# Performance work log

Hardware: AMD Instinct MI355X
Metric: run time of the kernel (lower is better)

## Reference

```python
import jax, jax.numpy as jnp
import numpy as np

T, B, N = 2048, 32, 1024   # time, batch, dan_hidden_size
H = 8                      # multihead_size
N2 = 128                   # attention_hidden_size
K = N // H                 # N_H = 128 per-head dim
K2 = N2 // H               # N2_H = 16 per-head attention dim


def setup_inputs() -> dict:
    key = jax.random.key(0)
    ks = jax.random.split(key, 10)
    s_n = 1.0 / np.sqrt(N)
    s_k = 1.0 / np.sqrt(K)
    s_k2 = 1.0 / np.sqrt(K2)
    return {
        "hyp": jax.random.normal(ks[0], (T, B, N), dtype=jnp.float32),
        # H independent per-head linears N -> K, stacked: (H, K, N)
        "Wmh": jax.random.uniform(ks[1], (H, K, N), minval=-s_n, maxval=s_n, dtype=jnp.float32),
        "bmh": jax.random.uniform(ks[2], (H, K), minval=-s_n, maxval=s_n, dtype=jnp.float32),
        # shared W: K -> K2
        "W": jax.random.uniform(ks[3], (K2, K), minval=-s_k, maxval=s_k, dtype=jnp.float32),
        "bW": jax.random.uniform(ks[4], (K2,), minval=-s_k, maxval=s_k, dtype=jnp.float32),
        # shared W_m: K -> K2
        "Wm": jax.random.uniform(ks[5], (K2, K), minval=-s_k, maxval=s_k, dtype=jnp.float32),
        "bWm": jax.random.uniform(ks[6], (K2,), minval=-s_k, maxval=s_k, dtype=jnp.float32),
        # shared W_h: K2 -> 1
        "Wh": jax.random.uniform(ks[7], (K2,), minval=-s_k2, maxval=s_k2, dtype=jnp.float32),
        "bWh": jax.random.uniform(ks[8], (), minval=-s_k2, maxval=s_k2, dtype=jnp.float32),
        "dan_hidden_size": N,
        "attention_hidden_size": N2,
        "multihead_size": H,
    }


def reference(hyp, Wmh, bmh, W, bW, Wm, bWm, Wh, bWh,
              dan_hidden_size, attention_hidden_size, multihead_size):
    # Per-head projections, all heads at once: (B, T, H, K)
    X = jnp.einsum('tbn,hkn->bthk', hyp, Wmh) + bmh
    # mean over time (original x.mean(0)): (B, H, K)
    m = X.mean(axis=1)
    # tanh-gated additive scoring: (B, T, H, K2)
    g = jnp.tanh(jnp.einsum('bthk,qk->bthq', X, W) + bW) \
        * jnp.tanh(jnp.einsum('bhk,qk->bhq', m, Wm) + bWm)[:, None]
    # scalar score per (b, t, h), softmax over time
    s = jnp.einsum('bthq,q->bth', g, Wh) + bWh
    a = jax.nn.softmax(s, axis=1)                       # (B, T, H)
    # attention-weighted sum over time: (B, H, K)
    c = jnp.einsum('bth,bthk->bhk', a, X)
    # concat heads along feature dim (head-major order, matches torch.cat)
    Bsz = c.shape[0]
    return c.reshape(Bsz, -1)                            # (B, N)
```

## Files before the change

kernel.cpp:

```cpp
#include <hip/hip_runtime.h>
#include <hip/hip_bf16.h>

#define T_DIM 2048
#define B_DIM 32
#define N_DIM 1024
#define H_DIM 8
#define K_DIM 128
#define Q_DIM 16

typedef __bf16 bf16x8 __attribute__((ext_vector_type(8)));
typedef __bf16 bf16x4 __attribute__((ext_vector_type(4)));
typedef float  f32x4  __attribute__((ext_vector_type(4)));

__device__ inline bf16x8 cvt8(float4 a, float4 b) {
    bf16x8 r;
    r[0] = (__bf16)a.x; r[1] = (__bf16)a.y; r[2] = (__bf16)a.z; r[3] = (__bf16)a.w;
    r[4] = (__bf16)b.x; r[5] = (__bf16)b.y; r[6] = (__bf16)b.z; r[7] = (__bf16)b.w;
    return r;
}

__global__ __launch_bounds__(256)
void cvt_f32_bf16(const float* __restrict__ s, __bf16* __restrict__ d)
{
    const long i = ((long)blockIdx.x * 256 + threadIdx.x) * 8;
    float4 a = *(const float4*)(s + i);
    float4 b = *(const float4*)(s + i + 4);
    *(bf16x8*)(d + i) = cvt8(a, b);
}

__global__ __launch_bounds__(512, 2)
void gemm_x_8ph(const __bf16* __restrict__ A, const __bf16* __restrict__ Bw,
                const float* __restrict__ bias, __bf16* __restrict__ X,
                float* __restrict__ mpart)
{
    __shared__ __bf16 lds[2][2][16384];

    const int tid  = threadIdx.x;
    const int lane = tid & 63;
    const int w    = tid >> 6;
    const int wm   = w >> 2;
    const int wn   = w & 3;

    const int bid  = blockIdx.x;
    const int wgid = (bid & 7) * 128 + (bid >> 3);
    const int bm   = wgid >> 2;
    const int bn   = wgid & 3;
    const long row0 = (long)bm * 256;
    const long col0 = (long)bn * 256;

    const int srow = w * 8 + (lane >> 3);
    const int scol = ((lane & 7) ^ (lane >> 3)) * 8;
    const __bf16* Ag = A  + (row0 + srow) * 1024 + scol;
    const __bf16* Bg = Bw + (col0 + srow) * 1024 + scol;
    const int ldst = w * 512;

    auto stage = [&](int kt, int sl) {
        const long ko = (long)kt * 64;
        #pragma unroll
        for (int j = 0; j < 4; ++j)
            __builtin_amdgcn_global_load_lds(
                (const __attribute__((address_space(1))) void*)(Ag + (long)j * 65536 + ko),
                (__attribute__((address_space(3))) void*)(&lds[sl][0][j * 4096 + ldst]),
                16, 0, 0);
        #pragma unroll
        for (int j = 0; j < 4; ++j)
            __builtin_amdgcn_global_load_lds(
                (const __attribute__((address_space(1))) void*)(Bg + (long)j * 65536 + ko),
                (__attribute__((address_space(3))) void*)(&lds[sl][1][j * 4096 + ldst]),
                16, 0, 0);
    };

    const int fr = lane & 15;
    const int g2 = lane >> 4;
    const int x7 = lane & 7;

    f32x4 acc[8][4];
    #pragma unroll
    for (int i = 0; i < 8; ++i)
        #pragma unroll
        for (int j = 0; j < 4; ++j)
            acc[i][j] = f32x4{0.f, 0.f, 0.f, 0.f};

    stage(0, 0);
    stage(1, 1);
    asm volatile("s_waitcnt vmcnt(8)" ::: "memory");
    __builtin_amdgcn_s_barrier();

    #pragma unroll 1
    for (int i = 0; i < 16; ++i) {
        const int s = i & 1;
        const __bf16* Al = &lds[s][0][0];
        const __bf16* Bl = &lds[s][1][0];

        bf16x8 a0[4], a0h[4], a1[4], a1h[4], b0[4], b1[4];

        #pragma unroll
        for (int mi = 0; mi < 4; ++mi) {
            const int row = wm * 128 + mi * 16 + fr;
            a0[mi] = *(const bf16x8*)(Al + row * 64 + ((g2) ^ x7) * 8);
        }
        #pragma unroll
        for (int ni = 0; ni < 4; ++ni) {
            const int row = wn * 64 + ni * 16 + fr;
            b0[ni] = *(const bf16x8*)(Bl + row * 64 + ((g2) ^ x7) * 8);
        }
        __builtin_amdgcn_s_barrier();
        __builtin_amdgcn_s_setprio(1);
        #pragma unroll
        for (int mi = 0; mi < 4; ++mi)
            #pragma unroll
            for (int ni = 0; ni < 4; ++ni)
                acc[mi][ni] = __builtin_amdgcn_mfma_f32_16x16x32_bf16(b0[ni], a0[mi], acc[mi][ni], 0, 0, 0);
        __builtin_amdgcn_s_setprio(0);
        __builtin_amdgcn_s_barrier();

        #pragma unroll
        for (int mi = 0; mi < 4; ++mi) {
            const int row = wm * 128 + mi * 16 + fr;
            a0h[mi] = *(const bf16x8*)(Al + row * 64 + ((4 + g2) ^ x7) * 8);
        }
        #pragma unroll
        for (int ni = 0; ni < 4; ++ni) {
            const int row = wn * 64 + ni * 16 + fr;
            b1[ni] = *(const bf16x8*)(Bl + row * 64 + ((4 + g2) ^ x7) * 8);
        }
        __builtin_amdgcn_s_barrier();
        __builtin_amdgcn_s_setprio(1);
        #pragma unroll
        for (int mi = 0; mi < 4; ++mi)
            #pragma unroll
            for (int ni = 0; ni < 4; ++ni)
                acc[mi][ni] = __builtin_amdgcn_mfma_f32_16x16x32_bf16(b1[ni], a0h[mi], acc[mi][ni], 0, 0, 0);
        __builtin_amdgcn_s_setprio(0);
        __builtin_amdgcn_s_barrier();

        #pragma unroll
        for (int mi = 0; mi < 4; ++mi) {
            const int row = wm * 128 + (mi + 4) * 16 + fr;
            a1[mi]  = *(const bf16x8*)(Al + row * 64 + ((g2    ) ^ x7) * 8);
            a1h[mi] = *(const bf16x8*)(Al + row * 64 + ((4 + g2) ^ x7) * 8);
        }
        __builtin_amdgcn_s_barrier();
        __builtin_amdgcn_s_setprio(1);
        #pragma unroll
        for (int mi = 0; mi < 4; ++mi)
            #pragma unroll
            for (int ni = 0; ni < 4; ++ni)
                acc[mi + 4][ni] = __builtin_amdgcn_mfma_f32_16x16x32_bf16(b0[ni], a1[mi], acc[mi + 4][ni], 0, 0, 0);
        __builtin_amdgcn_s_setprio(0);
        __builtin_amdgcn_s_barrier();

        if (i < 14) stage(i + 2, s);
        __builtin_amdgcn_s_barrier();
        __builtin_amdgcn_s_setprio(1);
        #pragma unroll
        for (int mi = 0; mi < 4; ++mi)
            #pragma unroll
            for (int ni = 0; ni < 4; ++ni)
                acc[mi + 4][ni] = __builtin_amdgcn_mfma_f32_16x16x32_bf16(b1[ni], a1h[mi], acc[mi + 4][ni], 0, 0, 0);
        __builtin_amdgcn_s_setprio(0);
        if (i < 14) { asm volatile("s_waitcnt vmcnt(8)" ::: "memory"); }
        else        { asm volatile("s_waitcnt vmcnt(0)" ::: "memory"); }
        __builtin_amdgcn_s_barrier();
    }

    const int g4 = lane >> 4;
    const long colb = col0 + wn * 64 + g4 * 4;

    float4 bias4[4];
    #pragma unroll
    for (int ni = 0; ni < 4; ++ni)
        bias4[ni] = *(const float4*)(bias + colb + ni * 16);

    f32x4 msum[2][4];
    #pragma unroll
    for (int bh = 0; bh < 2; ++bh)
        #pragma unroll
        for (int ni = 0; ni < 4; ++ni)
            msum[bh][ni] = f32x4{0.f, 0.f, 0.f, 0.f};

    #pragma unroll
    for (int mi = 0; mi < 8; ++mi) {
        const long row = row0 + wm * 128 + mi * 16 + fr;
        #pragma unroll
        for (int ni = 0; ni < 4; ++ni) {
            f32x4 xv;
            xv[0] = acc[mi][ni][0] + bias4[ni].x;
            xv[1] = acc[mi][ni][1] + bias4[ni].y;
            xv[2] = acc[mi][ni][2] + bias4[ni].z;
            xv[3] = acc[mi][ni][3] + bias4[ni].w;
            bf16x4 xb;
            xb[0] = (__bf16)xv[0]; xb[1] = (__bf16)xv[1];
            xb[2] = (__bf16)xv[2]; xb[3] = (__bf16)xv[3];
            *(bf16x4*)(X + row * 1024 + colb + ni * 16) = xb;
            msum[mi & 1][ni] += xv;
        }
    }

    float* ldsf = (float*)&lds[0][0][0];
    __syncthreads();
    if (wm == 1) {
        #pragma unroll
        for (int bh = 0; bh < 2; ++bh)
            #pragma unroll
            for (int ni = 0; ni < 4; ++ni)
                *(f32x4*)(ldsf + (bh * 16 + fr) * 256 + wn * 64 + ni * 16 + g4 * 4) = msum[bh][ni];
    }
    __syncthreads();
    if (wm == 0) {
        #pragma unroll
        for (int bh = 0; bh < 2; ++bh) {
            const int b = bh * 16 + fr;
            #pragma unroll
            for (int ni = 0; ni < 4; ++ni) {
                f32x4 other = *(const f32x4*)(ldsf + b * 256 + wn * 64 + ni * 16 + g4 * 4);
                f32x4 tot = msum[bh][ni] + other;
                *(f32x4*)(mpart + ((long)bm * 32 + b) * 1024 + colb + ni * 16) = tot;
            }
        }
    }
}

__global__ __launch_bounds__(256)
void gate2_k(const float* __restrict__ mpart, const float* __restrict__ Wm,
             const float* __restrict__ bWm, float* __restrict__ g2)
{
    __shared__ float mrow[1024];
    const int b = blockIdx.x;
    const int j4 = threadIdx.x * 4;
    f32x4 s = f32x4{0.f, 0.f, 0.f, 0.f};
    for (int bm = 0; bm < 256; ++bm)
        s += *(const f32x4*)(mpart + ((long)bm * 32 + b) * 1024 + j4);
    mrow[j4 + 0] = s[0] * (1.0f / 2048.0f);
    mrow[j4 + 1] = s[1] * (1.0f / 2048.0f);
    mrow[j4 + 2] = s[2] * (1.0f / 2048.0f);
    mrow[j4 + 3] = s[3] * (1.0f / 2048.0f);
    __syncthreads();
    if (threadIdx.x < 128) {
        const int h = threadIdx.x >> 4;
        const int q = threadIdx.x & 15;
        float d = bWm[q];
        #pragma unroll 8
        for (int k = 0; k < 128; ++k) d += mrow[h * 128 + k] * Wm[q * 128 + k];
        g2[(b * 8 + h) * 16 + q] = tanhf(d);
    }
}

__global__ __launch_bounds__(256)
void scores_k(const __bf16* __restrict__ X, const float* __restrict__ W,
              const float* __restrict__ bW, const float* __restrict__ g2,
              const float* __restrict__ Wh, const float* __restrict__ bWh,
              float* __restrict__ sbuf)
{
    const int tid   = threadIdx.x;
    const int lane  = tid & 63;
    const int w     = tid >> 6;
    const int gw    = blockIdx.x * 4 + w;
    const int rbase = gw * 16;
    const int q     = lane & 15;
    const int g4    = lane >> 4;

    bf16x8 bfr[4];
    #pragma unroll
    for (int c = 0; c < 4; ++c) {
        const float* wp = W + q * 128 + c * 32 + g4 * 8;
        float4 w0 = *(const float4*)wp;
        float4 w1 = *(const float4*)(wp + 4);
        bfr[c] = cvt8(w0, w1);
    }
    const __bf16* xp = X + (long)(rbase + q) * 128 + g4 * 8;
    bf16x8 afr[4];
    #pragma unroll
    for (int c = 0; c < 4; ++c) afr[c] = *(const bf16x8*)(xp + c * 32);

    f32x4 acc = f32x4{0.f, 0.f, 0.f, 0.f};
    #pragma unroll
    for (int c = 0; c < 4; ++c)
        acc = __builtin_amdgcn_mfma_f32_16x16x32_bf16(afr[c], bfr[c], acc, 0, 0, 0);

    const float whq  = Wh[q];
    const float bWv  = bW[q];
    const float bWhv = *bWh;
    #pragma unroll
    for (int r = 0; r < 4; ++r) {
        const int row = rbase + g4 * 4 + r;
        const int h   = row & 7;
        const int bt  = row >> 3;
        const int b   = bt & 31;
        const int t   = bt >> 5;
        float val = tanhf(acc[r] + bWv) * g2[(b * 8 + h) * 16 + q] * whq;
        val += __shfl_xor(val, 1);
        val += __shfl_xor(val, 2);
        val += __shfl_xor(val, 4);
        val += __shfl_xor(val, 8);
        if (q == 0) sbuf[(b * 8 + h) * 2048 + t] = val + bWhv;
    }
}

__global__ __launch_bounds__(256)
void softmax_k(float* __restrict__ s)
{
    __shared__ float red[256];
    const int bh = blockIdx.x;
    const int tid = threadIdx.x;
    float* row = s + bh * 2048;
    float4 v0 = *(const float4*)(row + tid * 8);
    float4 v1 = *(const float4*)(row + tid * 8 + 4);
    float v[8] = {v0.x, v0.y, v0.z, v0.w, v1.x, v1.y, v1.z, v1.w};
    float mx = v[0];
    #pragma unroll
    for (int i = 1; i < 8; ++i) mx = fmaxf(mx, v[i]);
    red[tid] = mx;
    __syncthreads();
    for (int st = 128; st > 0; st >>= 1) {
        if (tid < st) red[tid] = fmaxf(red[tid], red[tid + st]);
        __syncthreads();
    }
    mx = red[0];
    __syncthreads();
    float sum = 0.f;
    #pragma unroll
    for (int i = 0; i < 8; ++i) { v[i] = expf(v[i] - mx); sum += v[i]; }
    red[tid] = sum;
    __syncthreads();
    for (int st = 128; st > 0; st >>= 1) {
        if (tid < st) red[tid] += red[tid + st];
        __syncthreads();
    }
    const float inv = 1.0f / red[0];
    *(float4*)(row + tid * 8)     = make_float4(v[0] * inv, v[1] * inv, v[2] * inv, v[3] * inv);
    *(float4*)(row + tid * 8 + 4) = make_float4(v[4] * inv, v[5] * inv, v[6] * inv, v[7] * inv);
}

__global__ __launch_bounds__(256)
void wsum_k(const float* __restrict__ a, const __bf16* __restrict__ X,
            float* __restrict__ wpart)
{
    __shared__ float pk[8 * 128];
    const int bx = blockIdx.x;
    const int tc = bx & 7;
    const int bh = bx >> 3;
    const int b  = bh >> 3;
    const int h  = bh & 7;
    const int tid = threadIdx.x;
    const int kq = tid & 31;
    const int tr = tid >> 5;
    const float* ar = a + bh * 2048 + tc * 256;
    float a0 = 0.f, a1 = 0.f, a2 = 0.f, a3 = 0.f;
    #pragma unroll 4
    for (int i = tr; i < 256; i += 8) {
        const int t = tc * 256 + i;
        const float av = ar[i];
        bf16x4 xv = *(const bf16x4*)(X + (long)(t * 32 + b) * 1024 + h * 128 + kq * 4);
        a0 += av * (float)xv[0];
        a1 += av * (float)xv[1];
        a2 += av * (float)xv[2];
        a3 += av * (float)xv[3];
    }
    pk[tr * 128 + kq * 4 + 0] = a0;
    pk[tr * 128 + kq * 4 + 1] = a1;
    pk[tr * 128 + kq * 4 + 2] = a2;
    pk[tr * 128 + kq * 4 + 3] = a3;
    __syncthreads();
    if (tid < 128) {
        float s2 = 0.f;
        #pragma unroll
        for (int r = 0; r < 8; ++r) s2 += pk[r * 128 + tid];
        wpart[(long)bx * 128 + tid] = s2;
    }
}

__global__ __launch_bounds__(256)
void wsum_fin(const float* __restrict__ wpart, float* __restrict__ out)
{
    const int idx = blockIdx.x * 256 + threadIdx.x;
    const int k  = idx & 127;
    const int bh = idx >> 7;
    const int b  = bh >> 3;
    const int h  = bh & 7;
    float s = 0.f;
    #pragma unroll
    for (int tc = 0; tc < 8; ++tc) s += wpart[(bh * 8 + tc) * 128 + k];
    out[b * 1024 + h * 128 + k] = s;
}

extern "C" void kernel_launch(void* const* d_in, const int* in_sizes, int n_in,
                              void* d_out, int out_size, void* d_ws, size_t ws_size,
                              hipStream_t stream)
{
    const float* hyp = (const float*)d_in[0];
    const float* Wmh = (const float*)d_in[1];
    const float* bmh = (const float*)d_in[2];
    const float* W   = (const float*)d_in[3];
    const float* bW  = (const float*)d_in[4];
    const float* Wm  = (const float*)d_in[5];
    const float* bWm = (const float*)d_in[6];
    const float* Wh  = (const float*)d_in[7];
    const float* bWh = (const float*)d_in[8];
    float* out = (float*)d_out;

    char* ws = (char*)d_ws;
    const size_t SZ_X   = 134217728;
    const size_t SZ_AB  = 134217728;
    const size_t SZ_BB  = 2097152;
    const size_t SZ_MP  = 33554432;
    const size_t SZ_G2  = 16384;
    const size_t SZ_SB  = 2097152;

    size_t off = 0;
    __bf16* X     = (__bf16*)(ws + off); off += SZ_X;
    __bf16* Ab    = (__bf16*)(ws + off); off += SZ_AB;
    __bf16* Bb    = (__bf16*)(ws + off); off += SZ_BB;
    float*  mpart = (float*) (ws + off); off += SZ_MP;
    float*  g2    = (float*) (ws + off); off += SZ_G2;
    float*  sbuf  = (float*) (ws + off); off += SZ_SB;
    float*  wpart = (float*) (ws + off);

    cvt_f32_bf16<<<32768, 256, 0, stream>>>(hyp, Ab);
    cvt_f32_bf16<<<512,   256, 0, stream>>>(Wmh, Bb);
    gemm_x_8ph<<<1024, 512, 0, stream>>>(Ab, Bb, bmh, X, mpart);
    gate2_k<<<32, 256, 0, stream>>>(mpart, Wm, bWm, g2);
    scores_k<<<8192, 256, 0, stream>>>(X, W, bW, g2, Wh, bWh, sbuf);
    softmax_k<<<256, 256, 0, stream>>>(sbuf);
    wsum_k<<<2048, 256, 0, stream>>>(sbuf, X, wpart);
    wsum_fin<<<128, 256, 0, stream>>>(wpart, out);
}
```

Baseline: 346.7 us.

## Software-pipeline LDS fragment loads across MFMA phases and cut barriers

Restructures the GEMM main loop so the LDS fragment reads for the next phase are issued before the current MFMA block, and the first fragments of the next K-tile are prefetched from the other LDS buffer at the end of each iteration. The number of workgroup barriers per iteration drops from about eight to two, with an explicit lgkmcnt wait before the global-to-LDS staging overwrites the current buffer. The aim is to hide LDS latency behind matrix-core work and reduce synchronisation stalls. It raises register pressure from the fragments held across iterations, and ordering mistakes could cause LDS races.

```diff
diff --git a/kernel.cpp b/kernel.cpp
--- a/kernel.cpp
+++ b/kernel.cpp
@@ -86,25 +86,33 @@
     asm volatile("s_waitcnt vmcnt(8)" ::: "memory");
     __builtin_amdgcn_s_barrier();
 
+    bf16x8 a0[4], b0[4];
+    {
+        const __bf16* Al = &lds[0][0][0];
+        const __bf16* Bl = &lds[0][1][0];
+        #pragma unroll
+        for (int mi = 0; mi < 4; ++mi)
+            a0[mi] = *(const bf16x8*)(Al + (wm * 128 + mi * 16 + fr) * 64 + ((g2) ^ x7) * 8);
+        #pragma unroll
+        for (int ni = 0; ni < 4; ++ni)
+            b0[ni] = *(const bf16x8*)(Bl + (wn * 64 + ni * 16 + fr) * 64 + ((g2) ^ x7) * 8);
+    }
+
     #pragma unroll 1
     for (int i = 0; i < 16; ++i) {
         const int s = i & 1;
         const __bf16* Al = &lds[s][0][0];
         const __bf16* Bl = &lds[s][1][0];
 
-        bf16x8 a0[4], a0h[4], a1[4], a1h[4], b0[4], b1[4];
-
-        #pragma unroll
-        for (int mi = 0; mi < 4; ++mi) {
-            const int row = wm * 128 + mi * 16 + fr;
-            a0[mi] = *(const bf16x8*)(Al + row * 64 + ((g2) ^ x7) * 8);
-        }
-        #pragma unroll
-        for (int ni = 0; ni < 4; ++ni) {
-            const int row = wn * 64 + ni * 16 + fr;
-            b0[ni] = *(const bf16x8*)(Bl + row * 64 + ((g2) ^ x7) * 8);
-        }
-        __builtin_amdgcn_s_barrier();
+        bf16x8 a0h[4], a1[4], a1h[4], b1[4];
+
+        #pragma unroll
+        for (int mi = 0; mi < 4; ++mi)
+            a0h[mi] = *(const bf16x8*)(Al + (wm * 128 + mi * 16 + fr) * 64 + ((4 + g2) ^ x7) * 8);
+        #pragma unroll
+        for (int ni = 0; ni < 4; ++ni)
+            b1[ni] = *(const bf16x8*)(Bl + (wn * 64 + ni * 16 + fr) * 64 + ((4 + g2) ^ x7) * 8);
+
         __builtin_amdgcn_s_setprio(1);
         #pragma unroll
         for (int mi = 0; mi < 4; ++mi)
@@ -112,27 +120,6 @@
             for (int ni = 0; ni < 4; ++ni)
                 acc[mi][ni] = __builtin_amdgcn_mfma_f32_16x16x32_bf16(b0[ni], a0[mi], acc[mi][ni], 0, 0, 0);
         __builtin_amdgcn_s_setprio(0);
-        __builtin_amdgcn_s_barrier();
-
-        #pragma unroll
-        for (int mi = 0; mi < 4; ++mi) {
-            const int row = wm * 128 + mi * 16 + fr;
-            a0h[mi] = *(const bf16x8*)(Al + row * 64 + ((4 + g2) ^ x7) * 8);
-        }
-        #pragma unroll
-        for (int ni = 0; ni < 4; ++ni) {
-            const int row = wn * 64 + ni * 16 + fr;
-            b1[ni] = *(const bf16x8*)(Bl + row * 64 + ((4 + g2) ^ x7) * 8);
-        }
-        __builtin_amdgcn_s_barrier();
-        __builtin_amdgcn_s_setprio(1);
-        #pragma unroll
-        for (int mi = 0; mi < 4; ++mi)
-            #pragma unroll
-            for (int ni = 0; ni < 4; ++ni)
-                acc[mi][ni] = __builtin_amdgcn_mfma_f32_16x16x32_bf16(b1[ni], a0h[mi], acc[mi][ni], 0, 0, 0);
-        __builtin_amdgcn_s_setprio(0);
-        __builtin_amdgcn_s_barrier();
 
         #pragma unroll
         for (int mi = 0; mi < 4; ++mi) {
@@ -140,7 +127,18 @@
             a1[mi]  = *(const bf16x8*)(Al + row * 64 + ((g2    ) ^ x7) * 8);
             a1h[mi] = *(const bf16x8*)(Al + row * 64 + ((4 + g2) ^ x7) * 8);
         }
+        __builtin_amdgcn_s_setprio(1);
+        #pragma unroll
+        for (int mi = 0; mi < 4; ++mi)
+            #pragma unroll
+            for (int ni = 0; ni < 4; ++ni)
+                acc[mi][ni] = __builtin_amdgcn_mfma_f32_16x16x32_bf16(b1[ni], a0h[mi], acc[mi][ni], 0, 0, 0);
+        __builtin_amdgcn_s_setprio(0);
+
+        asm volatile("s_waitcnt lgkmcnt(0)" ::: "memory");
         __builtin_amdgcn_s_barrier();
+        if (i < 14) stage(i + 2, s);
+
         __builtin_amdgcn_s_setprio(1);
         #pragma unroll
         for (int mi = 0; mi < 4; ++mi)
@@ -148,20 +146,28 @@
             for (int ni = 0; ni < 4; ++ni)
                 acc[mi + 4][ni] = __builtin_amdgcn_mfma_f32_16x16x32_bf16(b0[ni], a1[mi], acc[mi + 4][ni], 0, 0, 0);
         __builtin_amdgcn_s_setprio(0);
-        __builtin_amdgcn_s_barrier();
-
-        if (i < 14) stage(i + 2, s);
-        __builtin_amdgcn_s_barrier();
-        __builtin_amdgcn_s_setprio(1);
-        #pragma unroll
-        for (int mi = 0; mi < 4; ++mi)
-            #pragma unroll
-            for (int ni = 0; ni < 4; ++ni)
-                acc[mi + 4][ni] = __builtin_amdgcn_mfma_f32_16x16x32_bf16(b1[ni], a1h[mi], acc[mi + 4][ni], 0, 0, 0);
-        __builtin_amdgcn_s_setprio(0);
+
         if (i < 14) { asm volatile("s_waitcnt vmcnt(8)" ::: "memory"); }
         else        { asm volatile("s_waitcnt vmcnt(0)" ::: "memory"); }
         __builtin_amdgcn_s_barrier();
+        if (i < 15) {
+            const __bf16* Aln = &lds[s ^ 1][0][0];
+            const __bf16* Bln = &lds[s ^ 1][1][0];
+            #pragma unroll
+            for (int mi = 0; mi < 4; ++mi)
+                a0[mi] = *(const bf16x8*)(Aln + (wm * 128 + mi * 16 + fr) * 64 + ((g2) ^ x7) * 8);
+            #pragma unroll
+            for (int ni = 0; ni < 4; ++ni)
+                b0[ni] = *(const bf16x8*)(Bln + (wn * 64 + ni * 16 + fr) * 64 + ((g2) ^ x7) * 8);
+        }
+
+        __builtin_amdgcn_s_setprio(1);
+        #pragma unroll
+        for (int mi = 0; mi < 4; ++mi)
+            #pragma unroll
+            for (int ni = 0; ni < 4; ++ni)
+                acc[mi + 4][ni] = __builtin_amdgcn_mfma_f32_16x16x32_bf16(b1[ni], a1h[mi], acc[mi + 4][ni], 0, 0, 0);
+        __builtin_amdgcn_s_setprio(0);
     }
 
     const int g4 = lane >> 4;
```

After: 329.5 us. -5.0%, faster.
